# Kernel tuning notes

Hardware: AMD Instinct MI355X
Metric: run time of the kernel (lower is better)

The kernel has to match this reference:

```python
import jax, jax.numpy as jnp
import numpy as np

V = 50000
E = 640000
DIM = 128
NUM_EDGE_TYPES = 32


def setup_inputs() -> dict:
    key = jax.random.key(0)
    ks = jax.random.split(key, 8)
    return {
        "node_values": jax.random.normal(ks[0], (V, DIM), dtype=jnp.float32),
        "edge_src": jax.random.randint(ks[1], (E,), 0, V, dtype=jnp.int32),
        "edge_dest": jax.random.randint(ks[2], (E,), 0, V, dtype=jnp.int32),
        "edge_cls": jax.random.randint(ks[3], (E,), 0, NUM_EDGE_TYPES, dtype=jnp.int32),
        "W_src": jax.random.normal(ks[4], (DIM, DIM), dtype=jnp.float32) / np.sqrt(DIM),
        "b_src": jnp.zeros((DIM,), dtype=jnp.float32),
        "W_dest": jax.random.normal(ks[5], (DIM, DIM), dtype=jnp.float32) / np.sqrt(DIM),
        "b_dest": jnp.zeros((DIM,), dtype=jnp.float32),
        "edge_emb": jax.random.normal(ks[6], (NUM_EDGE_TYPES, DIM), dtype=jnp.float32),
    }


def reference(node_values, edge_src, edge_dest, edge_cls, W_src, b_src, W_dest, b_dest, edge_emb):
    # Dense projections over all nodes, then gather per edge (matches tf.gather(dense(...), idx))
    src_proj = node_values @ W_src + b_src    # [V, dim]
    dest_proj = node_values @ W_dest + b_dest  # [V, dim]
    # Per-edge fused message: gather src, gather dest, edge-class embedding lookup, add, relu
    msgs = jax.nn.relu(src_proj[edge_src] + dest_proj[edge_dest] + edge_emb[edge_cls])  # [E, dim]
    # Scatter-reduce messages onto destination nodes
    out = jax.ops.segment_sum(msgs, edge_dest, num_segments=V)  # [V, dim]
    return out
```

## Files before the change

kernel.cpp:

```cpp
#include <hip/hip_runtime.h>


#define V 50000
#define E 640000
#define DIM 128
#define NXCD 8
#define NBIN_R 50
#define BINW 125
#define NBINS 400
#define CSTRIDE 16
#define BINCAP 2048
#define QCAP 384
#define NCHUNK 256
#define CSRN 2500
#define EC4 625
#define NPROJ 782
#define NFUSED 1038
#define SPAD 133

#define WFENCE() asm volatile("s_waitcnt lgkmcnt(0)" ::: "memory")

typedef __bf16 bf16x8 __attribute__((ext_vector_type(8)));
typedef float  f32x4  __attribute__((ext_vector_type(4)));
typedef float  f32x2  __attribute__((ext_vector_type(2)));

__device__ __forceinline__ float bf2f(unsigned int u16) {
    union { unsigned int i; float f; } c; c.i = u16 << 16; return c.f;
}
__device__ __forceinline__ unsigned int f2bf(float f) {
    union { float f; unsigned int i; } c; c.f = f;
    unsigned int u = c.i;
    return (u + 0x7FFFu + ((u >> 16) & 1u)) >> 16;
}

__global__ __launch_bounds__(256) void mp_setup(
    const float* __restrict__ Ws, const float* __restrict__ Wd,
    const float* __restrict__ emb,
    unsigned short* __restrict__ Wpk, unsigned short* __restrict__ embB,
    int* __restrict__ binCnt)
{
    int tid = blockIdx.x * 256 + threadIdx.x;
    int mat  = tid >> 11;
    int rem  = tid & 2047;
    int ct   = rem >> 8;
    int kt   = (rem >> 6) & 3;
    int lane = rem & 63;
    const float* W = mat ? Wd : Ws;
    int n  = ct * 16 + (lane & 15);
    int k0 = kt * 32 + (lane >> 4) * 8;
    unsigned short* dst = Wpk + (size_t)tid * 8;
    #pragma unroll
    for (int j = 0; j < 8; ++j) dst[j] = (unsigned short)f2bf(W[(k0 + j) * DIM + n]);
    embB[tid] = (unsigned short)f2bf(emb[tid]);
    for (int i = tid; i < NBINS * CSTRIDE; i += 4096) binCnt[i] = 0;
}

__global__ __launch_bounds__(256, 4) void mp_fused(
    const int* __restrict__ ed, const int* __restrict__ es, const int* __restrict__ ec,
    int* __restrict__ binCnt, int* __restrict__ binbuf,
    const float* __restrict__ x, const unsigned short* __restrict__ Wpk,
    const float* __restrict__ bs, const float* __restrict__ bd,
    unsigned char* __restrict__ ps8, unsigned short* __restrict__ pdB)
{
    __shared__ float stage[4][16 * SPAD];

    const int b = blockIdx.x;
    const int t = threadIdx.x;
    const bool isBin = ((b & 3) == 3) && (b < 1024);

    if (isBin) {
        int* base  = (int*)&stage[0][0];
        int* hist  = base;
        int* lofs  = base + 400;
        int* lcur  = base + 801;
        int* gbase = base + 1201;
        int* csr   = base + 1601;
        unsigned short* sbin = (unsigned short*)(base + 4101);

        const int c = b >> 2;

        for (int i = t; i < NBINS; i += 256) hist[i] = 0;

        int4 DV[3], SV[3], CV[3];
        {
            const int4* ed4 = (const int4*)ed + (size_t)c * EC4;
            const int4* es4 = (const int4*)es + (size_t)c * EC4;
            const int4* ec4 = (const int4*)ec + (size_t)c * EC4;
            #pragma unroll
            for (int k = 0; k < 3; ++k) {
                int i = t + k * 256;
                if (i < EC4) { DV[k] = ed4[i]; SV[k] = es4[i]; CV[k] = ec4[i]; }
                else { DV[k] = make_int4(-1, -1, -1, -1);
                       SV[k] = make_int4(0, 0, 0, 0); CV[k] = make_int4(0, 0, 0, 0); }
            }
        }
        __syncthreads();

        #pragma unroll
        for (int k = 0; k < 3; ++k) {
            #define H1(D) if ((D) >= 0) atomicAdd(&hist[(unsigned)(D) / BINW], 1);
            H1(DV[k].x); H1(DV[k].y); H1(DV[k].z); H1(DV[k].w);
            #undef H1
        }
        __syncthreads();

        for (int i = t; i < NBINS; i += 256)
            gbase[i] = atomicAdd(&binCnt[i * CSTRIDE], hist[i]);
        if (t < 64) {
            int carry = 0;
            #pragma unroll
            for (int s = 0; s < 7; ++s) {
                int idx = s * 64 + t;
                int v = (idx < NBINS) ? hist[idx] : 0;
                #pragma unroll
                for (int dlt = 1; dlt < 64; dlt <<= 1) {
                    int u = __shfl_up(v, dlt, 64);
                    if (t >= dlt) v += u;
                }
                int tot = __shfl(v, 63, 64);
                v += carry;
                if (idx < NBINS) { lofs[idx + 1] = v; lcur[idx] = v - hist[idx]; }
                carry += tot;
            }
            if (t == 0) lofs[0] = 0;
        }
        __syncthreads();

        #pragma unroll
        for (int k = 0; k < 3; ++k) {
            #define SC1(D, S, C) if ((D) >= 0) { \
                int bn = (unsigned)(D) / BINW; \
                int rl = (D) - bn * BINW; \
                int pos = atomicAdd(&lcur[bn], 1); \
                csr[pos] = ((S) & 0xFFFF) | ((C) << 16) | (rl << 21); \
                sbin[pos] = (unsigned short)bn; }
            SC1(DV[k].x, SV[k].x, CV[k].x); SC1(DV[k].y, SV[k].y, CV[k].y);
            SC1(DV[k].z, SV[k].z, CV[k].z); SC1(DV[k].w, SV[k].w, CV[k].w);
            #undef SC1
        }
        __syncthreads();

        for (int i = t; i < CSRN; i += 256) {
            int bb = sbin[i];
            int slot = gbase[bb] + (i - lofs[bb]);
            if (slot < BINCAP)
                binbuf[(size_t)bb * BINCAP + slot] = csr[i];
        }
        return;
    }

    const int p = (b < 1024) ? (b - ((b + 1) >> 2)) : (b - 256);
    if (p >= NPROJ) return;
    const int wave = __builtin_amdgcn_readfirstlane(threadIdx.x) >> 6;
    const int lane = threadIdx.x & 63;
    const int m = lane & 15, q = lane >> 4;
    const int row0 = p * 64 + wave * 16;

    int arow = row0 + m; if (arow >= V) arow = V - 1;
    const float* xr = x + (size_t)arow * DIM + q * 8;

    const bf16x8* Bp = (const bf16x8*)Wpk;

    bf16x8 b0[4], b1[4], b2[4];
    #pragma unroll
    for (int kt = 0; kt < 4; ++kt) b0[kt] = Bp[(0 * 32 + 0 * 4 + kt) * 64 + lane];
    #pragma unroll
    for (int kt = 0; kt < 4; ++kt) b1[kt] = Bp[(0 * 32 + 1 * 4 + kt) * 64 + lane];

    bf16x8 A[4];
    #pragma unroll
    for (int kt = 0; kt < 4; ++kt) {
        float4 u = *(const float4*)(xr + kt * 32);
        float4 v = *(const float4*)(xr + kt * 32 + 4);
        bf16x8 a;
        a[0] = (__bf16)u.x; a[1] = (__bf16)u.y; a[2] = (__bf16)u.z; a[3] = (__bf16)u.w;
        a[4] = (__bf16)v.x; a[5] = (__bf16)v.y; a[6] = (__bf16)v.z; a[7] = (__bf16)v.w;
        A[kt] = a;
    }

    float* st = stage[wave];
    const int rr = lane & 15, cg = lane >> 4;
    const int orow = row0 + rr;
    const float* rowp = st + rr * SPAD + cg * 32;

    {
        f32x4 acc[8];
        #pragma unroll
        for (int ct = 0; ct < 8; ++ct) {
            if (ct < 6) {
                #pragma unroll
                for (int kt = 0; kt < 4; ++kt)
                    b2[kt] = Bp[(0 * 32 + (ct + 2) * 4 + kt) * 64 + lane];
            }
            f32x4 a = {0.f, 0.f, 0.f, 0.f};
            #pragma unroll
            for (int kt = 0; kt < 4; ++kt)
                a = __builtin_amdgcn_mfma_f32_16x16x32_bf16(A[kt], b0[kt], a, 0, 0, 0);
            acc[ct] = a;
            #pragma unroll
            for (int kt = 0; kt < 4; ++kt) { b0[kt] = b1[kt]; b1[kt] = b2[kt]; }
        }

        #pragma unroll
        for (int kt = 0; kt < 4; ++kt) b0[kt] = Bp[(1 * 32 + 0 * 4 + kt) * 64 + lane];
        #pragma unroll
        for (int kt = 0; kt < 4; ++kt) b1[kt] = Bp[(1 * 32 + 1 * 4 + kt) * 64 + lane];

        #pragma unroll
        for (int ct = 0; ct < 8; ++ct) {
            const float bv = bs[ct * 16 + m];
            #pragma unroll
            for (int rg = 0; rg < 4; ++rg)
                st[(q * 4 + rg) * SPAD + ct * 16 + m] = acc[ct][rg] + bv;
        }
    }
    WFENCE();
    {
        int w[8];
        #pragma unroll
        for (int j = 0; j < 8; ++j) {
            float4 f = *(const float4*)(rowp + 4 * j);
            int v = __builtin_amdgcn_cvt_pk_fp8_f32(f.x, f.y, 0, false);
            v = __builtin_amdgcn_cvt_pk_fp8_f32(f.z, f.w, v, true);
            w[j] = v;
        }
        if (orow < V) {
            int4* dst = (int4*)(ps8 + (size_t)orow * 128 + cg * 32);
            dst[0] = make_int4(w[0], w[1], w[2], w[3]);
            dst[1] = make_int4(w[4], w[5], w[6], w[7]);
        }
    }
    WFENCE();

    {
        f32x4 acc[8];
        #pragma unroll
        for (int ct = 0; ct < 8; ++ct) {
            if (ct < 6) {
                #pragma unroll
                for (int kt = 0; kt < 4; ++kt)
                    b2[kt] = Bp[(1 * 32 + (ct + 2) * 4 + kt) * 64 + lane];
            }
            f32x4 a = {0.f, 0.f, 0.f, 0.f};
            #pragma unroll
            for (int kt = 0; kt < 4; ++kt)
                a = __builtin_amdgcn_mfma_f32_16x16x32_bf16(A[kt], b0[kt], a, 0, 0, 0);
            acc[ct] = a;
            #pragma unroll
            for (int kt = 0; kt < 4; ++kt) { b0[kt] = b1[kt]; b1[kt] = b2[kt]; }
        }
        #pragma unroll
        for (int ct = 0; ct < 8; ++ct) {
            const float bv = bd[ct * 16 + m];
            #pragma unroll
            for (int rg = 0; rg < 4; ++rg)
                st[(q * 4 + rg) * SPAD + ct * 16 + m] = acc[ct][rg] + bv;
        }
    }
    WFENCE();
    {
        int w[16];
        #pragma unroll
        for (int j = 0; j < 8; ++j) {
            float4 f = *(const float4*)(rowp + 4 * j);
            w[2 * j]     = f2bf(f.x) | (f2bf(f.y) << 16);
            w[2 * j + 1] = f2bf(f.z) | (f2bf(f.w) << 16);
        }
        if (orow < V) {
            int4* dst = (int4*)(pdB + (size_t)orow * 128 + cg * 32);
            #pragma unroll
            for (int jj = 0; jj < 4; ++jj)
                dst[jj] = make_int4(w[4 * jj], w[4 * jj + 1], w[4 * jj + 2], w[4 * jj + 3]);
        }
    }
}

__global__ __launch_bounds__(256) void mp_binBC(
    const unsigned char* __restrict__ ps8, const unsigned short* __restrict__ pdB,
    const unsigned short* __restrict__ embB,
    const int* __restrict__ binCnt, const int* __restrict__ binbuf,
    float* __restrict__ out)
{
    __shared__ int csr[QCAP];
    __shared__ int cnt[16];
    __shared__ int off[17];
    __shared__ int cur[16];
    __shared__ unsigned short sEmb[32 * DIM];

    const int r = blockIdx.x & (NXCD - 1);
    const int rest = blockIdx.x >> 3;
    const int bi = rest % NBIN_R;
    const int qu = rest / NBIN_R;
    const int bin = r * NBIN_R + bi;
    const int rel0 = qu * 16;
    const int relW = (qu == 7) ? 13 : 16;
    const int d0 = bin * BINW + rel0;
    const int t = threadIdx.x;
    const int wave = t >> 6, lane = t & 63;

    int nb = binCnt[bin * CSTRIDE]; if (nb > BINCAP) nb = BINCAP;
    const int* buf = binbuf + (size_t)bin * BINCAP;

    if (t < 16) cnt[t] = 0;

    {
        const int4* s4 = (const int4*)embB;
        int4* d4 = (int4*)sEmb;
        d4[t] = s4[t];
        d4[t + 256] = s4[t + 256];
    }

    int EB[8];
    #pragma unroll
    for (int k = 0; k < 8; ++k) {
        int i = t + k * 256;
        EB[k] = (i < nb) ? buf[i] : -1;
    }

    float dp0v[4], dp1v[4];
    #pragma unroll
    for (int k = 0; k < 4; ++k) {
        int rl = wave + k * 4;
        int d = d0 + ((rl < relW) ? rl : 0);
        unsigned int pdu = *(const unsigned int*)(pdB + (size_t)d * DIM + 2 * lane);
        dp0v[k] = bf2f(pdu & 0xFFFF); dp1v[k] = bf2f(pdu >> 16);
    }
    __syncthreads();

    #pragma unroll
    for (int k = 0; k < 8; ++k) {
        int rl = (int)((unsigned)EB[k] >> 21) - rel0;
        if ((unsigned)rl < (unsigned)relW) atomicAdd(&cnt[rl], 1);
    }
    __syncthreads();

    if (t < 16) {
        int v = (t < relW) ? cnt[t] : 0;
        #pragma unroll
        for (int dlt = 1; dlt < 16; dlt <<= 1) {
            int u = __shfl_up(v, dlt, 64);
            if (t >= dlt) v += u;
        }
        off[t + 1] = v;
        cur[t] = v - cnt[t];
        if (t == 0) off[0] = 0;
    }
    __syncthreads();

    #pragma unroll
    for (int k = 0; k < 8; ++k) {
        int rl = (int)((unsigned)EB[k] >> 21) - rel0;
        if ((unsigned)rl < (unsigned)relW) {
            int pos = atomicAdd(&cur[rl], 1);
            if (pos < QCAP) csr[pos] = EB[k];
        }
    }
    __syncthreads();

    #define PROC(P) { \
        int s_ = *(const unsigned short*)(ps8 + ((size_t)((P) & 0xFFFF) << 7) + 2 * lane); \
        unsigned int e_ = *(const unsigned int*)(sEmb + ((((P) >> 16) & 0x1F) << 7) + 2 * lane); \
        f32x2 f_ = __builtin_amdgcn_cvt_pk_f32_fp8(s_, false); \
        a0 += fmaxf(f_.x + dp0 + bf2f(e_ & 0xFFFF), 0.f); \
        a1 += fmaxf(f_.y + dp1 + bf2f(e_ >> 16),    0.f); }

    #pragma unroll
    for (int k = 0; k < 4; ++k) {
        const int rl = wave + k * 4;
        if (rl >= relW) break;
        const int d = d0 + rl;
        int i0 = off[rl], i1 = off[rl + 1];
        if (i1 > QCAP) i1 = QCAP;
        if (i0 > i1) i0 = i1;
        const float dp0 = dp0v[k], dp1 = dp1v[k];
        float a0 = 0.f, a1 = 0.f;
        int i = i0;
        for (; i + 8 <= i1; i += 8) {
            int p0 = csr[i],     p1 = csr[i + 1], p2 = csr[i + 2], p3 = csr[i + 3];
            int p4 = csr[i + 4], p5 = csr[i + 5], p6 = csr[i + 6], p7 = csr[i + 7];
            PROC(p0); PROC(p1); PROC(p2); PROC(p3);
            PROC(p4); PROC(p5); PROC(p6); PROC(p7);
        }
        for (; i + 4 <= i1; i += 4) {
            int p0 = csr[i], p1 = csr[i + 1], p2 = csr[i + 2], p3 = csr[i + 3];
            PROC(p0); PROC(p1); PROC(p2); PROC(p3);
        }
        for (; i < i1; ++i) { int p0 = csr[i]; PROC(p0); }
        *(float2*)(out + (size_t)d * DIM + 2 * lane) = make_float2(a0, a1);
    }
    #undef PROC
}

extern "C" void kernel_launch(void* const* d_in, const int* in_sizes, int n_in,
                              void* d_out, int out_size, void* d_ws, size_t ws_size,
                              hipStream_t stream) {
    const float* x   = (const float*)d_in[0];
    const int*   es  = (const int*)d_in[1];
    const int*   ed  = (const int*)d_in[2];
    const int*   ec  = (const int*)d_in[3];
    const float* Ws  = (const float*)d_in[4];
    const float* bs  = (const float*)d_in[5];
    const float* Wd  = (const float*)d_in[6];
    const float* bd  = (const float*)d_in[7];
    const float* emb = (const float*)d_in[8];
    float* out = (float*)d_out;

    char* ws = (char*)d_ws;
    size_t off = 0;
    unsigned char*  ps8  = (unsigned char*)(ws + off);  off += (size_t)V * 128;
    unsigned short* pdB  = (unsigned short*)(ws + off); off += (size_t)V * DIM * 2;
    int* binbuf = (int*)(ws + off);                     off += (size_t)NBINS * BINCAP * 4;
    int* binCnt = (int*)(ws + off);                     off += (size_t)NBINS * CSTRIDE * 4;
    unsigned short* Wpk  = (unsigned short*)(ws + off); off += 2 * 128 * 128 * 2;
    unsigned short* embB = (unsigned short*)(ws + off); off += 32 * 128 * 2;

    mp_setup<<<16, 256, 0, stream>>>(Ws, Wd, emb, Wpk, embB, binCnt);
    mp_fused<<<NFUSED, 256, 0, stream>>>(ed, es, ec, binCnt, binbuf,
                                         x, Wpk, bs, bd, ps8, pdB);
    mp_binBC<<<NBIN_R * NXCD * 8, 256, 0, stream>>>(ps8, pdB, embB, binCnt, binbuf, out);
}
```

Before: 136.4 us.

## Process whole destination bin per 512-thread block instead of eight sub-blocks

The gather/reduce kernel now launches one 512-thread block per bin (400 blocks) instead of eight 256-thread blocks per bin, each handling 16 destination rows. Each block reads the bin's edge list once, builds a full 125-row CSR in shared memory, and each wave loops over about 16 rows. This removes the eightfold redundant reading and filtering of the bin buffer and embedding copy, at the cost of far fewer blocks (400 on a 256-CU device), a serialized per-wave row loop, and the XCD-aware block mapping being dropped.

```diff
diff --git a/kernel.cpp b/kernel.cpp
--- a/kernel.cpp
+++ b/kernel.cpp
@@ -4,13 +4,11 @@
 #define V 50000
 #define E 640000
 #define DIM 128
-#define NXCD 8
 #define NBIN_R 50
 #define BINW 125
 #define NBINS 400
 #define CSTRIDE 16
 #define BINCAP 2048
-#define QCAP 384
 #define NCHUNK 256
 #define CSRN 2500
 #define EC4 625
@@ -275,84 +273,71 @@
     }
 }
 
-__global__ __launch_bounds__(256) void mp_binBC(
+__global__ __launch_bounds__(512) void mp_binBC(
     const unsigned char* __restrict__ ps8, const unsigned short* __restrict__ pdB,
     const unsigned short* __restrict__ embB,
     const int* __restrict__ binCnt, const int* __restrict__ binbuf,
     float* __restrict__ out)
 {
-    __shared__ int csr[QCAP];
-    __shared__ int cnt[16];
-    __shared__ int off[17];
-    __shared__ int cur[16];
+    __shared__ int csr[BINCAP];
+    __shared__ int cnt[128];
+    __shared__ int off2[129];
+    __shared__ int cur[128];
     __shared__ unsigned short sEmb[32 * DIM];
 
-    const int r = blockIdx.x & (NXCD - 1);
-    const int rest = blockIdx.x >> 3;
-    const int bi = rest % NBIN_R;
-    const int qu = rest / NBIN_R;
-    const int bin = r * NBIN_R + bi;
-    const int rel0 = qu * 16;
-    const int relW = (qu == 7) ? 13 : 16;
-    const int d0 = bin * BINW + rel0;
+    const int bin = blockIdx.x;
+    const int d0 = bin * BINW;
     const int t = threadIdx.x;
     const int wave = t >> 6, lane = t & 63;
 
     int nb = binCnt[bin * CSTRIDE]; if (nb > BINCAP) nb = BINCAP;
     const int* buf = binbuf + (size_t)bin * BINCAP;
 
-    if (t < 16) cnt[t] = 0;
-
-    {
-        const int4* s4 = (const int4*)embB;
-        int4* d4 = (int4*)sEmb;
-        d4[t] = s4[t];
-        d4[t + 256] = s4[t + 256];
-    }
-
-    int EB[8];
-    #pragma unroll
-    for (int k = 0; k < 8; ++k) {
-        int i = t + k * 256;
+    if (t < 128) cnt[t] = 0;
+
+    ((int4*)sEmb)[t] = ((const int4*)embB)[t];
+
+    int EB[4];
+    #pragma unroll
+    for (int k = 0; k < 4; ++k) {
+        int i = t + k * 512;
         EB[k] = (i < nb) ? buf[i] : -1;
     }
-
-    float dp0v[4], dp1v[4];
+    __syncthreads();
+
     #pragma unroll
     for (int k = 0; k < 4; ++k) {
-        int rl = wave + k * 4;
-        int d = d0 + ((rl < relW) ? rl : 0);
-        unsigned int pdu = *(const unsigned int*)(pdB + (size_t)d * DIM + 2 * lane);
-        dp0v[k] = bf2f(pdu & 0xFFFF); dp1v[k] = bf2f(pdu >> 16);
+        unsigned int rl = (unsigned)EB[k] >> 21;
+        if (rl < (unsigned)BINW) atomicAdd(&cnt[rl], 1);
     }
     __syncthreads();
 
-    #pragma unroll
-    for (int k = 0; k < 8; ++k) {
-        int rl = (int)((unsigned)EB[k] >> 21) - rel0;
-        if ((unsigned)rl < (unsigned)relW) atomicAdd(&cnt[rl], 1);
+    if (t < 64) {
+        int carry = 0;
+        #pragma unroll
+        for (int s = 0; s < 2; ++s) {
+            int idx = s * 64 + t;
+            int v = (idx < BINW) ? cnt[idx] : 0;
+            #pragma unroll
+            for (int dlt = 1; dlt < 64; dlt <<= 1) {
+                int u = __shfl_up(v, dlt, 64);
+                if (t >= dlt) v += u;
+            }
+            int tot = __shfl(v, 63, 64);
+            v += carry;
+            if (idx < BINW) { off2[idx + 1] = v; cur[idx] = v - cnt[idx]; }
+            carry += tot;
+        }
+        if (t == 0) off2[0] = 0;
     }
     __syncthreads();
 
-    if (t < 16) {
-        int v = (t < relW) ? cnt[t] : 0;
-        #pragma unroll
-        for (int dlt = 1; dlt < 16; dlt <<= 1) {
-            int u = __shfl_up(v, dlt, 64);
-            if (t >= dlt) v += u;
-        }
-        off[t + 1] = v;
-        cur[t] = v - cnt[t];
-        if (t == 0) off[0] = 0;
-    }
-    __syncthreads();
-
-    #pragma unroll
-    for (int k = 0; k < 8; ++k) {
-        int rl = (int)((unsigned)EB[k] >> 21) - rel0;
-        if ((unsigned)rl < (unsigned)relW) {
+    #pragma unroll
+    for (int k = 0; k < 4; ++k) {
+        unsigned int rl = (unsigned)EB[k] >> 21;
+        if (rl < (unsigned)BINW) {
             int pos = atomicAdd(&cur[rl], 1);
-            if (pos < QCAP) csr[pos] = EB[k];
+            csr[pos] = EB[k];
         }
     }
     __syncthreads();
@@ -365,14 +350,13 @@
         a1 += fmaxf(f_.y + dp1 + bf2f(e_ >> 16),    0.f); }
 
     #pragma unroll
-    for (int k = 0; k < 4; ++k) {
-        const int rl = wave + k * 4;
-        if (rl >= relW) break;
+    for (int k = 0; k < 16; ++k) {
+        const int rl = wave + k * 8;
+        if (rl >= BINW) break;
         const int d = d0 + rl;
-        int i0 = off[rl], i1 = off[rl + 1];
-        if (i1 > QCAP) i1 = QCAP;
-        if (i0 > i1) i0 = i1;
-        const float dp0 = dp0v[k], dp1 = dp1v[k];
+        unsigned int pdu = *(const unsigned int*)(pdB + (size_t)d * DIM + 2 * lane);
+        const float dp0 = bf2f(pdu & 0xFFFF), dp1 = bf2f(pdu >> 16);
+        int i0 = off2[rl], i1 = off2[rl + 1];
         float a0 = 0.f, a1 = 0.f;
         int i = i0;
         for (; i + 8 <= i1; i += 8) {
@@ -417,5 +401,5 @@
     mp_setup<<<16, 256, 0, stream>>>(Ws, Wd, emb, Wpk, embB, binCnt);
     mp_fused<<<NFUSED, 256, 0, stream>>>(ed, es, ec, binCnt, binbuf,
                                          x, Wpk, bs, bd, ps8, pdB);
-    mp_binBC<<<NBIN_R * NXCD * 8, 256, 0, stream>>>(ps8, pdB, embB, binCnt, binbuf, out);
-}
+    mp_binBC<<<NBINS, 512, 0, stream>>>(ps8, pdB, embB, binCnt, binbuf, out);
+}
```

Result: slower. 148.6 us (+8.9%).
